# Performance work log

Hardware: AMD Instinct MI355X
Metric: run time of the kernel (lower is better)

Reference implementation:

```python
import jax, jax.numpy as jnp
import numpy as np
from functools import partial

B, N, NCLS = 16, 25200, 80
M_TGT = 50
MAX_DET = 300
CONF_THRES = 0.8
NMS_THRES = 0.4


def cxcywh_to_xyxy(boxes):
    # cxcywh -> xywh -> xyxy (as in tensor_to_dict: cxcywh_to_xywh then xywh_to_xyxy)
    cx, cy, w, h = boxes[..., 0], boxes[..., 1], boxes[..., 2], boxes[..., 3]
    x1 = cx - 0.5 * w
    y1 = cy - 0.5 * h
    return jnp.stack([x1, y1, x1 + w, y1 + h], axis=-1)


def pairwise_iou(b):
    # b: [K,4] xyxy
    x1 = jnp.maximum(b[:, None, 0], b[None, :, 0])
    y1 = jnp.maximum(b[:, None, 1], b[None, :, 1])
    x2 = jnp.minimum(b[:, None, 2], b[None, :, 2])
    y2 = jnp.minimum(b[:, None, 3], b[None, :, 3])
    inter = jnp.clip(x2 - x1, 0.0) * jnp.clip(y2 - y1, 0.0)
    area = jnp.clip(b[:, 2] - b[:, 0], 0.0) * jnp.clip(b[:, 3] - b[:, 1], 0.0)
    return inter / (area[:, None] + area[None, :] - inter + 1e-9)


def nms_one(boxes_xyxy, labels, valid):
    # boxes sorted by score descending; class-aware greedy NMS, fixed K iterations
    K = boxes_xyxy.shape[0]
    iou = pairwise_iou(boxes_xyxy)
    same = labels[:, None] == labels[None, :]
    supp = (iou > NMS_THRES) & same
    idx = jnp.arange(K)

    def body(i, keep):
        kill = supp[i] & (idx > i) & keep[i]
        return keep & ~kill

    return jax.lax.fori_loop(0, K, body, valid)


def post_process(preds):
    # preds: [B, N, 5+C] (cx,cy,w,h,obj,cls...)
    obj = preds[..., 4]
    cls_prob = preds[..., 5:]
    cls_conf = jnp.max(cls_prob, axis=-1)
    cls_id = jnp.argmax(cls_prob, axis=-1)
    score = obj * cls_conf                      # [B,N]
    score = jnp.where(score > CONF_THRES, score, 0.0)
    top_s, top_i = jax.lax.top_k(score, MAX_DET)            # [B,K]
    boxes = jnp.take_along_axis(preds[..., :4], top_i[..., None], axis=1)  # cxcywh [B,K,4]
    labels = jnp.take_along_axis(cls_id, top_i, axis=1)     # [B,K]
    valid = top_s > 0.0
    boxes_xyxy = cxcywh_to_xyxy(boxes)
    keep = jax.vmap(nms_one)(boxes_xyxy, labels, valid)     # [B,K]
    scores = jnp.where(keep, top_s, 0.0)
    boxes_xyxy = jnp.where(keep[..., None], boxes_xyxy, 0.0)
    labels = jnp.where(keep, labels, -1)
    return boxes_xyxy, scores, labels, keep


def process_targets(tt, lengths):
    # tt: [B, M, 6] = cxcywh, score, label ; lengths: [B]
    valid = jnp.arange(tt.shape[1])[None, :] < lengths[:, None]  # [B,M]
    boxes = cxcywh_to_xyxy(tt[..., :4])
    scores = tt[..., 4]
    labels = tt[..., 5].astype(jnp.int32)
    boxes = jnp.where(valid[..., None], boxes, 0.0)
    scores = jnp.where(valid, scores, 0.0)
    labels = jnp.where(valid, labels, -1)
    return boxes, scores, labels, valid


def setup_inputs() -> dict:
    key = jax.random.key(0)
    k1, k2, k3, k4 = jax.random.split(key, 4)
    preds = jax.random.uniform(k1, (B, N, 5 + NCLS), dtype=jnp.float32)
    tgt_boxes = jax.random.uniform(k2, (B, M_TGT, 4), dtype=jnp.float32) * 640.0
    tgt_scores = jnp.ones((B, M_TGT, 1), dtype=jnp.float32)
    tgt_labels = jax.random.randint(k3, (B, M_TGT, 1), 0, NCLS).astype(jnp.float32)
    target_target = jnp.concatenate([tgt_boxes, tgt_scores, tgt_labels], axis=-1)
    target_lengths = jax.random.randint(k4, (B,), 1, M_TGT + 1).astype(jnp.int32)
    return {"preds": preds, "target_target": target_target, "target_lengths": target_lengths}


def reference(preds, target_target, target_lengths):
    pb, ps, pl, pv = post_process(preds)
    tb, ts, tl, tv = process_targets(target_target, target_lengths)
    # @torch.no_grad in original forward
    out = (pb, ps, pl, pv, tb, ts, tl, tv)
    return jax.tree_util.tree_map(jax.lax.stop_gradient, out)
```

## Files before the change

### kernel.cpp

```cpp
#include <hip/hip_runtime.h>
#include <cstdint>

#define BB 16
#define NN 25200
#define NCLS 80
#define NF (5 + NCLS)
#define MAXDET 300
#define MTGT 50
#define CONF 0.8f
#define NMSTH 0.4f
#define WORDS 10
#define NBINS 2048
#define SBUF 2048
#define APB 64
#define CHUNK_V4 (APB * NF / 4)
#define SCORE_BLOCKS ((BB * NN) / APB)
#define NTGT_BLOCKS ((BB * MTGT + 127) / 128)
#define HSTRIDE 33

#define WS_SCORE 0
#define WS_DS   ((size_t)BB * NN * 4)
#define WS_DI   (WS_DS + (size_t)BB * MAXDET * 4)
#define WS_GBOX (WS_DI + (size_t)BB * MAXDET * 4)
#define WS_GLAB (WS_GBOX + (size_t)BB * MAXDET * 16)

#define O_PB 0
#define O_PS (BB * MAXDET * 4)
#define O_PL (O_PS + BB * MAXDET)
#define O_PV (O_PL + BB * MAXDET)
#define O_TB (O_PV + BB * MAXDET)
#define O_TS (O_TB + BB * MTGT * 4)
#define O_TL (O_TS + BB * MTGT)
#define O_TV (O_TL + BB * MTGT)

__global__ __launch_bounds__(128) void k_score(const float* __restrict__ preds,
                                               float* __restrict__ scores,
                                               const float* __restrict__ tt,
                                               const int* __restrict__ len,
                                               float* __restrict__ out) {
    __shared__ float st[APB * NF];
    int tid = threadIdx.x;
    int bid = blockIdx.x;

    if (bid >= SCORE_BLOCKS) {
        int t = (bid - SCORE_BLOCKS) * 128 + tid;
        if (t < BB * MTGT) {
            int b = t / MTGT, m = t - b * MTGT;
            const float* row = tt + (size_t)t * 6;
            bool valid = m < len[b];
            float cx = row[0], cy = row[1], w = row[2], h = row[3];
            float x1 = cx - 0.5f * w, y1 = cy - 0.5f * h;
            float* tb = out + O_TB + (size_t)t * 4;
            tb[0] = valid ? x1 : 0.f;
            tb[1] = valid ? y1 : 0.f;
            tb[2] = valid ? (x1 + w) : 0.f;
            tb[3] = valid ? (y1 + h) : 0.f;
            out[O_TS + t] = valid ? row[4] : 0.f;
            out[O_TL + t] = valid ? (float)(int)row[5] : -1.f;
            out[O_TV + t] = valid ? 1.f : 0.f;
        }
        return;
    }

    int w = tid >> 6;
    const float4* src = (const float4*)(preds + (size_t)bid * (APB * NF));
    #pragma unroll
    for (int i = 0; i < 11; ++i) {
        int idx = i * 128 + tid;
        if (idx < CHUNK_V4) {
            __builtin_amdgcn_global_load_lds(
                (const __attribute__((address_space(1))) void*)(src + idx),
                (__attribute__((address_space(3))) void*)(st + (i * 128 + w * 64) * 4),
                16, 0, 0);
        }
    }
    __syncthreads();

    int a = tid >> 1, h = tid & 1;
    const float* cls = st + a * NF + 5 + h * 40;
    float m0 = cls[0], m1 = cls[1], m2 = cls[2], m3 = cls[3];
    #pragma unroll
    for (int f = 4; f < 40; f += 4) {
        m0 = fmaxf(m0, cls[f]);     m1 = fmaxf(m1, cls[f + 1]);
        m2 = fmaxf(m2, cls[f + 2]); m3 = fmaxf(m3, cls[f + 3]);
    }
    float m = fmaxf(fmaxf(m0, m1), fmaxf(m2, m3));
    m = fmaxf(m, __shfl_xor(m, 1));
    if (h == 0) scores[bid * APB + a] = st[a * NF + 4] * m;
}

__global__ __launch_bounds__(1024) void k_select(const float* __restrict__ scores,
                                                 float* __restrict__ dscore,
                                                 unsigned* __restrict__ didx) {
    __shared__ int hist[64 * HSTRIDE];
    __shared__ unsigned long long sk[SBUF];
    __shared__ int lcnt;
    __shared__ int scut;
    int b = blockIdx.x;
    int tid = threadIdx.x;
    int lane = tid & 63;

    if (tid == 0) lcnt = 0;
    for (int i = tid; i < 64 * HSTRIDE; i += 1024) hist[i] = 0;
    for (int i = tid; i < SBUF; i += 1024) sk[i] = 0ull;
    __syncthreads();

    for (int i = tid; i < NN; i += 1024) {
        float s = scores[b * NN + i];
        if (s > CONF) {
            unsigned u = __float_as_uint(s);
            int bin = (int)((u - 0x3F400000u) >> 12);
            bin = bin < 0 ? 0 : (bin > NBINS - 1 ? NBINS - 1 : bin);
            atomicAdd(&hist[(bin >> 5) * HSTRIDE + (bin & 31)], 1);
        }
    }
    __syncthreads();

    if (tid < 64) {
        int sb = 0;
        #pragma unroll
        for (int k = 0; k < 32; ++k) sb += hist[lane * HSTRIDE + k];
        int cum = sb;
        #pragma unroll
        for (int d = 1; d < 64; d <<= 1) {
            int o = __shfl_down(cum, d);
            if (lane + d < 64) cum += o;
        }
        unsigned long long m = __ballot(cum >= MAXDET);
        int cutbin = 0;
        if (m) {
            int cutS = 63 - __clzll(m);
            int tail = (cutS < 63) ? __shfl(cum, cutS + 1) : 0;
            int hh = (lane < 32) ? hist[cutS * HSTRIDE + lane] : 0;
            int c2 = hh;
            #pragma unroll
            for (int d = 1; d < 32; d <<= 1) {
                int o = __shfl_down(c2, d);
                if (lane + d < 32) c2 += o;
            }
            c2 += tail;
            unsigned long long m2 = __ballot(lane < 32 && c2 >= MAXDET);
            int cutL = 63 - __clzll(m2);
            cutbin = cutS * 32 + cutL;
        }
        if (lane == 0) scut = cutbin;
    }
    __syncthreads();
    int cutbin = scut;

    for (int i = tid; i < ((NN + 1023) & ~1023); i += 1024) {
        float s = 0.f; bool pass = false;
        if (i < NN) {
            s = scores[b * NN + i];
            if (s > CONF) {
                unsigned u = __float_as_uint(s);
                int bin = (int)((u - 0x3F400000u) >> 12);
                bin = bin < 0 ? 0 : (bin > NBINS - 1 ? NBINS - 1 : bin);
                pass = bin >= cutbin;
            }
        }
        unsigned long long mask = __ballot(pass);
        int wcnt = __popcll(mask);
        int bs = 0;
        if (lane == 0 && wcnt) bs = atomicAdd(&lcnt, wcnt);
        bs = __shfl(bs, 0);
        if (pass) {
            int pos = bs + __popcll(mask & ((1ull << lane) - 1ull));
            if (pos < SBUF)
                sk[pos] = ((unsigned long long)__float_as_uint(s) << 32) |
                          (unsigned long long)(0xFFFFFFFFu - (unsigned)i);
        }
    }
    __syncthreads();

    int M = lcnt; if (M > SBUF) M = SBUF;
    unsigned P = 512;
    while ((int)P < M) P <<= 1;

    for (unsigned k = 2; k <= P; k <<= 1) {
        for (unsigned j = k >> 1; j > 0; j >>= 1) {
            __syncthreads();
            for (unsigned i = tid; i < P; i += 1024) {
                unsigned ixj = i ^ j;
                if (ixj > i) {
                    unsigned long long a = sk[i], d = sk[ixj];
                    bool desc = ((i & k) == 0);
                    if (desc ? (a < d) : (a > d)) { sk[i] = d; sk[ixj] = a; }
                }
            }
        }
    }
    __syncthreads();
    for (int q = tid; q < MAXDET; q += 1024) {
        unsigned long long key = sk[q];
        unsigned sbits = (unsigned)(key >> 32);
        dscore[b * MAXDET + q] = __uint_as_float(sbits);
        didx[b * MAXDET + q]   = sbits ? (0xFFFFFFFFu - (unsigned)(key & 0xFFFFFFFFu)) : 0u;
    }
}

__global__ __launch_bounds__(512) void k_gather(const float* __restrict__ preds,
                                                const float* __restrict__ dscore,
                                                const unsigned* __restrict__ didx,
                                                float* __restrict__ gbox,
                                                int* __restrict__ glabel) {
    int g    = blockIdx.x * 8 + (threadIdx.x >> 6);
    int lane = threadIdx.x & 63;
    float sc = dscore[g];
    if (sc > 0.f) {
        int b = g / MAXDET;
        int idx = (int)didx[g];
        const float* row = preds + ((size_t)b * NN + (size_t)idx) * NF;
        float v = row[5 + lane]; int ci = lane;
        if (lane < 16) { float v2 = row[69 + lane]; if (v2 > v) { v = v2; ci = lane + 64; } }
        #pragma unroll
        for (int m = 32; m >= 1; m >>= 1) {
            float ov = __shfl_xor(v, m);
            int   oi = __shfl_xor(ci, m);
            if (ov > v || (ov == v && oi < ci)) { v = ov; ci = oi; }
        }
        if (lane == 0) {
            float cx = row[0], cy = row[1], w = row[2], h = row[3];
            float x1 = cx - 0.5f * w, y1 = cy - 0.5f * h;
            float4 bx = { x1, y1, x1 + w, y1 + h };
            ((float4*)gbox)[g] = bx;
            glabel[g] = ci;
        }
    } else if (lane == 0) {
        float4 zz = { 0.f, 0.f, 0.f, 0.f };
        ((float4*)gbox)[g] = zz;
        glabel[g] = -1;
    }
}

__global__ __launch_bounds__(1024) void k_nms2(const float* __restrict__ gbox,
                                               const int* __restrict__ glabel,
                                               const float* __restrict__ dscore,
                                               float* __restrict__ out) {
    __shared__ float4   sbox[MAXDET];
    __shared__ int      slabel[MAXDET];
    __shared__ float    sscore[MAXDET];
    __shared__ unsigned supp[MAXDET * WORDS];
    int b = blockIdx.x;
    int tid = threadIdx.x;

    if (tid < MAXDET) {
        int g = b * MAXDET + tid;
        sbox[tid]   = ((const float4*)gbox)[g];
        slabel[tid] = glabel[g];
        sscore[tid] = dscore[g];
    }
    __syncthreads();

    for (int T = tid; T < MAXDET * WORDS; T += 1024) {
        int i  = T / WORDS;
        int jw = T - i * WORDS;
        unsigned word = 0;
        int jbase = jw * 32;
        if (jbase + 31 > i) {
            float4 bi = sbox[i];
            int   li = slabel[i];
            float si = sscore[i];
            float ai = __fmul_rn(fmaxf(__fsub_rn(bi.z, bi.x), 0.f),
                                 fmaxf(__fsub_rn(bi.w, bi.y), 0.f));
            for (int uu = 0; uu < 32; ++uu) {
                int t = (uu + jw) & 31;
                int j = jbase + t;
                if (j > i && j < MAXDET) {
                    if (slabel[j] == li && si > 0.f && sscore[j] > 0.f) {
                        float4 bj = sbox[j];
                        float xx1 = fmaxf(bi.x, bj.x);
                        float yy1 = fmaxf(bi.y, bj.y);
                        float xx2 = fminf(bi.z, bj.z);
                        float yy2 = fminf(bi.w, bj.w);
                        float iw = fmaxf(__fsub_rn(xx2, xx1), 0.f);
                        float ih = fmaxf(__fsub_rn(yy2, yy1), 0.f);
                        float inter = __fmul_rn(iw, ih);
                        float aj = __fmul_rn(fmaxf(__fsub_rn(bj.z, bj.x), 0.f),
                                             fmaxf(__fsub_rn(bj.w, bj.y), 0.f));
                        float den = __fadd_rn(__fsub_rn(__fadd_rn(ai, aj), inter), 1e-9f);
                        float iou = inter / den;
                        if (iou > NMSTH) word |= 1u << t;
                    }
                }
            }
        }
        supp[T] = word;
    }
    __syncthreads();

    if (tid < 64) {
        int lane = tid;
        unsigned keep = 0, nzm = 0;
        #pragma unroll
        for (int s = 0; s < 5; ++s) {
            int k = s * 64 + lane;
            bool kb = (k < MAXDET) && (sscore[k] > 0.f);
            unsigned long long m = __ballot(kb);
            if (lane == 2 * s)     keep = (unsigned)m;
            if (lane == 2 * s + 1) keep = (unsigned)(m >> 32);
            unsigned nz = 0;
            if (k < MAXDET) {
                #pragma unroll
                for (int w = 0; w < WORDS; ++w) nz |= supp[k * WORDS + w];
            }
            unsigned long long mn = __ballot(nz != 0u);
            if (lane == 2 * s)     nzm = (unsigned)mn;
            if (lane == 2 * s + 1) nzm = (unsigned)(mn >> 32);
        }

        for (int i = 0; i < MAXDET; ++i) {
            int idx = i >> 5;
            unsigned kw = __shfl(keep, idx);
            unsigned nw = __shfl(nzm, idx);
            if (((kw & nw) >> (i & 31)) & 1u) {
                if (lane < WORDS) keep &= ~supp[i * WORDS + lane];
            }
        }

        #pragma unroll
        for (int s = 0; s < 5; ++s) {
            int k = s * 64 + lane;
            if (k < MAXDET) {
                unsigned kw = __shfl(keep, k >> 5);
                bool kp = (kw >> (k & 31)) & 1u;
                int g = b * MAXDET + k;
                float4 bx = sbox[k];
                float4 zz = { 0.f, 0.f, 0.f, 0.f };
                ((float4*)(out + O_PB))[g] = kp ? bx : zz;
                out[O_PS + g] = kp ? sscore[k] : 0.f;
                out[O_PL + g] = kp ? (float)slabel[k] : -1.f;
                out[O_PV + g] = kp ? 1.f : 0.f;
            }
        }
    }
}

extern "C" void kernel_launch(void* const* d_in, const int* in_sizes, int n_in,
                              void* d_out, int out_size, void* d_ws, size_t ws_size,
                              hipStream_t stream) {
    const float* preds = (const float*)d_in[0];
    const float* tt    = (const float*)d_in[1];
    const int*   len   = (const int*)d_in[2];
    float* out = (float*)d_out;

    char* ws = (char*)d_ws;
    float*    scores = (float*)(ws + WS_SCORE);
    float*    dscore = (float*)(ws + WS_DS);
    unsigned* didx   = (unsigned*)(ws + WS_DI);
    float*    gbox   = (float*)(ws + WS_GBOX);
    int*      glabel = (int*)(ws + WS_GLAB);

    k_score <<<SCORE_BLOCKS + NTGT_BLOCKS, 128, 0, stream>>>(preds, scores, tt, len, out);
    k_select<<<BB, 1024, 0, stream>>>(scores, dscore, didx);
    k_gather<<<(BB * MAXDET) / 8, 512, 0, stream>>>(preds, dscore, didx, gbox, glabel);
    k_nms2  <<<BB, 1024, 0, stream>>>(gbox, glabel, dscore, out);
}
```

Measured before the change: 96.41 us.

## Split per-batch top-k selection into multi-block histogram, filter and sort kernels

The single-block-per-batch select kernel is split into a 256-block histogram pass with global atomics, a 256-block filter pass that compacts candidates above the cut bin into a global key buffer, and a per-batch bitonic sort kernel. Each batch is spread over 16 blocks, so far more of the GPU is busy than with 16 blocks total. The cost is three extra kernel launches, including a zeroing kernel, and global atomics plus workspace round trips. Candidate order in the key buffer now depends on atomic timing, and the sort restores a deterministic order.

```diff
diff --git a/kernel.cpp b/kernel.cpp
--- a/kernel.cpp
+++ b/kernel.cpp
@@ -12,6 +12,9 @@
 #define WORDS 10
 #define NBINS 2048
 #define SBUF 2048
+#define CAPK 8192
+#define SLICE 1575
+#define LCAP 1600
 #define APB 64
 #define CHUNK_V4 (APB * NF / 4)
 #define SCORE_BLOCKS ((BB * NN) / APB)
@@ -19,7 +22,10 @@
 #define HSTRIDE 33
 
 #define WS_SCORE 0
-#define WS_DS   ((size_t)BB * NN * 4)
+#define WS_HIST ((size_t)BB * NN * 4)
+#define WS_CNT  (WS_HIST + (size_t)BB * NBINS * 4)
+#define WS_KEYS (WS_CNT + 1024)
+#define WS_DS   (WS_KEYS + (size_t)BB * CAPK * 8)
 #define WS_DI   (WS_DS + (size_t)BB * MAXDET * 4)
 #define WS_GBOX (WS_DI + (size_t)BB * MAXDET * 4)
 #define WS_GLAB (WS_GBOX + (size_t)BB * MAXDET * 16)
@@ -32,6 +38,13 @@
 #define O_TS (O_TB + BB * MTGT * 4)
 #define O_TL (O_TS + BB * MTGT)
 #define O_TV (O_TL + BB * MTGT)
+
+__global__ __launch_bounds__(1024) void k_zero(int* __restrict__ ghist,
+                                               int* __restrict__ cnt) {
+    int i = blockIdx.x * 1024 + threadIdx.x;
+    if (i < BB * NBINS) ghist[i] = 0;
+    if (i < 256) cnt[i] = 0;
+}
 
 __global__ __launch_bounds__(128) void k_score(const float* __restrict__ preds,
                                                float* __restrict__ scores,
@@ -89,31 +102,44 @@
     if (h == 0) scores[bid * APB + a] = st[a * NF + 4] * m;
 }
 
-__global__ __launch_bounds__(1024) void k_select(const float* __restrict__ scores,
-                                                 float* __restrict__ dscore,
-                                                 unsigned* __restrict__ didx) {
+__global__ __launch_bounds__(1024) void k_hist(const float* __restrict__ scores,
+                                               int* __restrict__ ghist) {
+    __shared__ int h[NBINS];
+    int b = blockIdx.x >> 4, s = blockIdx.x & 15;
+    int tid = threadIdx.x;
+    for (int i = tid; i < NBINS; i += 1024) h[i] = 0;
+    __syncthreads();
+    const float* base = scores + (size_t)b * NN + s * SLICE;
+    for (int i = tid; i < SLICE; i += 1024) {
+        float v = base[i];
+        if (v > CONF) {
+            unsigned u = __float_as_uint(v);
+            int bin = (int)((u - 0x3F400000u) >> 12);
+            bin = bin < 0 ? 0 : (bin > NBINS - 1 ? NBINS - 1 : bin);
+            atomicAdd(&h[bin], 1);
+        }
+    }
+    __syncthreads();
+    for (int i = tid; i < NBINS; i += 1024) {
+        int v = h[i];
+        if (v) atomicAdd(&ghist[b * NBINS + i], v);
+    }
+}
+
+__global__ __launch_bounds__(1024) void k_filter(const float* __restrict__ scores,
+                                                 const int* __restrict__ ghist,
+                                                 int* __restrict__ cnt,
+                                                 unsigned long long* __restrict__ keys) {
     __shared__ int hist[64 * HSTRIDE];
-    __shared__ unsigned long long sk[SBUF];
-    __shared__ int lcnt;
-    __shared__ int scut;
-    int b = blockIdx.x;
+    __shared__ unsigned long long sloc[LCAP];
+    __shared__ int lc, gbase, scut;
+    int b = blockIdx.x >> 4, s = blockIdx.x & 15;
     int tid = threadIdx.x;
     int lane = tid & 63;
 
-    if (tid == 0) lcnt = 0;
-    for (int i = tid; i < 64 * HSTRIDE; i += 1024) hist[i] = 0;
-    for (int i = tid; i < SBUF; i += 1024) sk[i] = 0ull;
-    __syncthreads();
-
-    for (int i = tid; i < NN; i += 1024) {
-        float s = scores[b * NN + i];
-        if (s > CONF) {
-            unsigned u = __float_as_uint(s);
-            int bin = (int)((u - 0x3F400000u) >> 12);
-            bin = bin < 0 ? 0 : (bin > NBINS - 1 ? NBINS - 1 : bin);
-            atomicAdd(&hist[(bin >> 5) * HSTRIDE + (bin & 31)], 1);
-        }
-    }
+    if (tid == 0) lc = 0;
+    for (int i = tid; i < NBINS; i += 1024)
+        hist[(i >> 5) * HSTRIDE + (i & 31)] = ghist[b * NBINS + i];
     __syncthreads();
 
     if (tid < 64) {
@@ -148,35 +174,48 @@
     __syncthreads();
     int cutbin = scut;
 
-    for (int i = tid; i < ((NN + 1023) & ~1023); i += 1024) {
-        float s = 0.f; bool pass = false;
-        if (i < NN) {
-            s = scores[b * NN + i];
-            if (s > CONF) {
-                unsigned u = __float_as_uint(s);
-                int bin = (int)((u - 0x3F400000u) >> 12);
-                bin = bin < 0 ? 0 : (bin > NBINS - 1 ? NBINS - 1 : bin);
-                pass = bin >= cutbin;
-            }
-        }
-        unsigned long long mask = __ballot(pass);
-        int wcnt = __popcll(mask);
-        int bs = 0;
-        if (lane == 0 && wcnt) bs = atomicAdd(&lcnt, wcnt);
-        bs = __shfl(bs, 0);
-        if (pass) {
-            int pos = bs + __popcll(mask & ((1ull << lane) - 1ull));
-            if (pos < SBUF)
-                sk[pos] = ((unsigned long long)__float_as_uint(s) << 32) |
-                          (unsigned long long)(0xFFFFFFFFu - (unsigned)i);
-        }
-    }
-    __syncthreads();
-
-    int M = lcnt; if (M > SBUF) M = SBUF;
+    const float* base = scores + (size_t)b * NN + s * SLICE;
+    for (int i = tid; i < SLICE; i += 1024) {
+        float v = base[i];
+        if (v > CONF) {
+            unsigned u = __float_as_uint(v);
+            int bin = (int)((u - 0x3F400000u) >> 12);
+            bin = bin < 0 ? 0 : (bin > NBINS - 1 ? NBINS - 1 : bin);
+            if (bin >= cutbin) {
+                int p = atomicAdd(&lc, 1);
+                if (p < LCAP) {
+                    unsigned aidx = (unsigned)(s * SLICE + i);
+                    sloc[p] = ((unsigned long long)u << 32) |
+                              (unsigned long long)(0xFFFFFFFFu - aidx);
+                }
+            }
+        }
+    }
+    __syncthreads();
+    int n = lc < LCAP ? lc : LCAP;
+    if (tid == 0) gbase = atomicAdd(&cnt[b * 16], n);
+    __syncthreads();
+    int gb = gbase;
+    for (int i = tid; i < n; i += 1024) {
+        int gp = gb + i;
+        if (gp < CAPK) keys[(size_t)b * CAPK + gp] = sloc[i];
+    }
+}
+
+__global__ __launch_bounds__(1024) void k_sel2(const int* __restrict__ cnt,
+                                               const unsigned long long* __restrict__ keys,
+                                               float* __restrict__ dscore,
+                                               unsigned* __restrict__ didx) {
+    __shared__ unsigned long long sk[SBUF];
+    int b = blockIdx.x;
+    int tid = threadIdx.x;
+    int M = cnt[b * 16]; if (M > SBUF) M = SBUF;
+
+    for (int i = tid; i < SBUF; i += 1024)
+        sk[i] = (i < M) ? keys[(size_t)b * CAPK + i] : 0ull;
+
     unsigned P = 512;
     while ((int)P < M) P <<= 1;
-
     for (unsigned k = 2; k <= P; k <<= 1) {
         for (unsigned j = k >> 1; j > 0; j >>= 1) {
             __syncthreads();
@@ -346,13 +385,19 @@
 
     char* ws = (char*)d_ws;
     float*    scores = (float*)(ws + WS_SCORE);
+    int*      ghist  = (int*)(ws + WS_HIST);
+    int*      cnt    = (int*)(ws + WS_CNT);
+    unsigned long long* keys = (unsigned long long*)(ws + WS_KEYS);
     float*    dscore = (float*)(ws + WS_DS);
     unsigned* didx   = (unsigned*)(ws + WS_DI);
     float*    gbox   = (float*)(ws + WS_GBOX);
     int*      glabel = (int*)(ws + WS_GLAB);
 
+    k_zero  <<<(BB * NBINS + 1023) / 1024, 1024, 0, stream>>>(ghist, cnt);
     k_score <<<SCORE_BLOCKS + NTGT_BLOCKS, 128, 0, stream>>>(preds, scores, tt, len, out);
-    k_select<<<BB, 1024, 0, stream>>>(scores, dscore, didx);
+    k_hist  <<<BB * 16, 1024, 0, stream>>>(scores, ghist);
+    k_filter<<<BB * 16, 1024, 0, stream>>>(scores, ghist, cnt, keys);
+    k_sel2  <<<BB, 1024, 0, stream>>>(cnt, keys, dscore, didx);
     k_gather<<<(BB * MAXDET) / 8, 512, 0, stream>>>(preds, dscore, didx, gbox, glabel);
     k_nms2  <<<BB, 1024, 0, stream>>>(gbox, glabel, dscore, out);
 }
```

Result: faster. 91.71 us (-4.9%).
